# Optimization experiments

Hardware: AMD Instinct MI355X
Metric: run time of the kernel (lower is better)

## Reference

```python
import math
import jax, jax.numpy as jnp
import numpy as np

B, S, H, NH = 2, 2048, 1024, 4
DH = H // NH


def setup_inputs() -> dict:
    key = jax.random.key(0)
    ks = jax.random.split(key, 8)
    gate_std = 1.0 / math.sqrt(3 * H)
    return {
        "q": jax.random.normal(ks[0], (B, S, H), jnp.float32),
        "k": jax.random.normal(ks[1], (B, S, H), jnp.float32),
        "v": jax.random.normal(ks[2], (B, S, H), jnp.float32),
        "w_igate": jax.random.normal(ks[3], (NH, 3 * H), jnp.float32) * gate_std,
        "b_igate": jax.random.normal(ks[4], (NH,), jnp.float32) * 0.1,
        "w_fgate": jax.random.normal(ks[5], (NH, 3 * H), jnp.float32) * gate_std,
        "b_fgate": jnp.linspace(3.4, 6.0, NH, dtype=jnp.float32),  # bias_linspace_init_
        "ln_weight": jnp.zeros((H,), jnp.float32),  # residual weight: effective scale = 1 + w
    }


def _mlstm_parallel(qh, kh, vh, ig, fg, eps=1e-6):
    # qh,kh,vh: (B,NH,S,DH); ig,fg: (B,NH,S)
    b, nh, s, dh = qh.shape
    log_f = jax.nn.log_sigmoid(fg)                       # (B,NH,S)
    pcs = jnp.pad(jnp.cumsum(log_f, axis=-1), ((0, 0), (0, 0), (1, 0)))  # (B,NH,S+1)
    mat = pcs[..., :, None] - pcs[..., None, :]          # (B,NH,S+1,S+1)
    ltr = jnp.tril(jnp.ones((s, s), dtype=bool))
    log_fg_matrix = jnp.where(ltr, mat[..., 1:, 1:], -jnp.inf)
    log_D = log_fg_matrix + ig[..., None, :]             # (B,NH,S,S)
    max_log_D = jnp.max(log_D, axis=-1, keepdims=True)   # rowwise stabilization
    D = jnp.exp(log_D - max_log_D)
    qk = jnp.einsum('bhsd,bhtd->bhst', qh, kh) / math.sqrt(dh)
    C = qk * D
    normalizer = jnp.maximum(jnp.abs(C.sum(axis=-1, keepdims=True)), jnp.exp(-max_log_D))
    Cn = C / (normalizer + eps)
    return jnp.einsum('bhst,bhtd->bhsd', Cn, vh)         # (B,NH,S,DH)


def reference(q, k, v, w_igate, b_igate, w_fgate, b_fgate, ln_weight):
    b, s, h = q.shape
    nh = b_igate.shape[0]
    dh = h // nh
    # gate preactivations from concat([q,k,v])
    gin = jnp.concatenate([q, k, v], axis=-1)            # (B,S,3H)
    ig = jnp.einsum('bsd,hd->bhs', gin, w_igate) + b_igate[None, :, None]
    fg = jnp.einsum('bsd,hd->bhs', gin, w_fgate) + b_fgate[None, :, None]
    # split heads
    qh = q.reshape(b, s, nh, dh).transpose(0, 2, 1, 3)
    kh = k.reshape(b, s, nh, dh).transpose(0, 2, 1, 3)
    vh = v.reshape(b, s, nh, dh).transpose(0, 2, 1, 3)
    hst = _mlstm_parallel(qh, kh, vh, ig, fg)            # (B,NH,S,DH)
    # MultiHeadLayerNorm: group_norm over DH per head (biased variance), scale = 1 + ln_weight
    mean = hst.mean(axis=-1, keepdims=True)
    var = hst.var(axis=-1, keepdims=True)
    hn = (hst - mean) / jnp.sqrt(var + 1e-5)
    scale = (1.0 + ln_weight).reshape(nh, dh)
    hn = hn * scale[None, :, None, :]
    return hn.transpose(0, 2, 1, 3).reshape(b, s, h)
```

## Files before the change

kernel.cpp:

```cpp
#include <hip/hip_runtime.h>
#include <hip/hip_bf16.h>
#include <cstddef>

constexpr int Bx = 2, Sx = 2048, Hx = 1024, NHx = 4, DHx = 256;
constexpr float RSQ = 0.0625f;

typedef __attribute__((ext_vector_type(8))) short    bf16x8;
typedef __attribute__((ext_vector_type(4))) float    f32x4;

__device__ __forceinline__ float logsigf(float x) {
  return (x >= 0.0f) ? -log1pf(expf(-x)) : x - log1pf(expf(x));
}
__device__ __forceinline__ unsigned short f2bf(float x) {
  unsigned u = __builtin_bit_cast(unsigned, x);
  u = (u + 0x7fffu + ((u >> 16) & 1u)) >> 16;
  return (unsigned short)u;
}
__device__ __forceinline__ unsigned pk2bf(float a, float b) {
  return (unsigned)f2bf(a) | ((unsigned)f2bf(b) << 16);
}

__global__ __launch_bounds__(256)
void gates_kernel(const float* __restrict__ q, const float* __restrict__ k,
                  const float* __restrict__ v,
                  const float* __restrict__ wi, const float* __restrict__ bi,
                  const float* __restrict__ wf, const float* __restrict__ bf,
                  float* __restrict__ ig, float* __restrict__ fg,
                  unsigned short* __restrict__ Qb, unsigned short* __restrict__ Kb)
{
  const int bs = blockIdx.x;
  const int t  = threadIdx.x;
  const int b = bs >> 11, spos = bs & 2047;
  float p[8] = {0,0,0,0,0,0,0,0};
  const size_t rowoff = (size_t)bs * Hx;
  for (int idx = t; idx < 3 * Hx; idx += 256) {
    float gv;
    if (idx < Hx) {
      gv = q[rowoff + idx];
      Qb[((size_t)(b * NHx + (idx >> 8)) * Sx + spos) * DHx + (idx & 255)] = f2bf(gv);
    } else if (idx < 2 * Hx) {
      gv = k[rowoff + idx - Hx];
      int kd = idx - Hx;
      Kb[((size_t)(b * NHx + (kd >> 8)) * Sx + spos) * DHx + (kd & 255)] = f2bf(gv);
    } else {
      gv = v[rowoff + idx - 2 * Hx];
    }
#pragma unroll
    for (int h = 0; h < NHx; ++h) {
      p[h]     += gv * wi[h * 3 * Hx + idx];
      p[4 + h] += gv * wf[h * 3 * Hx + idx];
    }
  }
  __shared__ float red[8][256];
#pragma unroll
  for (int g2 = 0; g2 < 8; ++g2) red[g2][t] = p[g2];
  __syncthreads();
  for (int s2 = 128; s2 > 0; s2 >>= 1) {
    if (t < s2) {
#pragma unroll
      for (int g2 = 0; g2 < 8; ++g2) red[g2][t] += red[g2][t + s2];
    }
    __syncthreads();
  }
  if (t < 8) {
    const int h = t & 3;
    const size_t o = ((size_t)(b * NHx + h)) * Sx + spos;
    if (t < 4) ig[o] = red[t][0] + bi[h];
    else       fg[o] = red[t][0] + bf[h];
  }
}

__global__ __launch_bounds__(256)
void scan_kernel(const float* __restrict__ ig, const float* __restrict__ fg,
                 float* __restrict__ av, float* __restrict__ Mv,
                 float* __restrict__ nfv)
{
  const int bh = blockIdx.x;
  const int t  = threadIdx.x;
  const size_t base = (size_t)bh * Sx;
  const int s0 = t * 8;
  float4 f0 = *(const float4*)(fg + base + s0);
  float4 f1 = *(const float4*)(fg + base + s0 + 4);
  float4 g0 = *(const float4*)(ig + base + s0);
  float4 g1 = *(const float4*)(ig + base + s0 + 4);
  float xf[8] = {f0.x,f0.y,f0.z,f0.w,f1.x,f1.y,f1.z,f1.w};
  float xi[8] = {g0.x,g0.y,g0.z,g0.w,g1.x,g1.y,g1.z,g1.w};
  float ps[8];
  float run = 0.0f;
#pragma unroll
  for (int i = 0; i < 8; ++i) { run += logsigf(xf[i]); ps[i] = run; }
  __shared__ float ssum[256];
  __shared__ float smax[256];
  ssum[t] = run;
  __syncthreads();
  for (int st = 1; st < 256; st <<= 1) {
    float addv = (t >= st) ? ssum[t - st] : 0.0f;
    __syncthreads();
    ssum[t] += addv;
    __syncthreads();
  }
  const float exs = (t > 0) ? ssum[t - 1] : 0.0f;
  float a[8], pm[8];
  float rm = -INFINITY;
#pragma unroll
  for (int i = 0; i < 8; ++i) {
    a[i] = xi[i] - (exs + ps[i]);
    rm = fmaxf(rm, a[i]);
    pm[i] = rm;
  }
  smax[t] = rm;
  __syncthreads();
  for (int st = 1; st < 256; st <<= 1) {
    float mv = (t >= st) ? smax[t - st] : -INFINITY;
    __syncthreads();
    smax[t] = fmaxf(smax[t], mv);
    __syncthreads();
  }
  const float exm = (t > 0) ? smax[t - 1] : -INFINITY;
#pragma unroll
  for (int i = 0; i < 8; ++i) {
    const float M = fmaxf(exm, pm[i]);
    const float F = exs + ps[i];
    av[base + s0 + i]  = a[i];
    Mv[base + s0 + i]  = M;
    nfv[base + s0 + i] = expf(-(F + M));
  }
}

__global__ __launch_bounds__(256)
void vtrans_kernel(const float* __restrict__ v, unsigned short* __restrict__ vt)
{
  __shared__ float tile[64][68];
  const int st0 = blockIdx.x * 64, dt0 = blockIdx.y * 64;
  const int bh = blockIdx.z, b = bh >> 2, h = bh & 3;
  const int t = threadIdx.x;
#pragma unroll
  for (int i = 0; i < 4; ++i) {
    int u = t + 256 * i;
    int r = u >> 4, c4 = (u & 15) * 4;
    const float* p = v + ((size_t)(b * Sx) + st0 + r) * Hx + h * DHx + dt0 + c4;
    float4 vv = *(const float4*)p;
    tile[r][c4] = vv.x; tile[r][c4+1] = vv.y; tile[r][c4+2] = vv.z; tile[r][c4+3] = vv.w;
  }
  __syncthreads();
#pragma unroll
  for (int i = 0; i < 4; ++i) {
    int u = t + 256 * i;
    int dr = u >> 4, c4 = (u & 15) * 4;
    ushort4 o;
    o.x = f2bf(tile[c4+0][dr]); o.y = f2bf(tile[c4+1][dr]);
    o.z = f2bf(tile[c4+2][dr]); o.w = f2bf(tile[c4+3][dr]);
    *(ushort4*)(vt + ((size_t)bh * DHx + dt0 + dr) * Sx + st0 + c4) = o;
  }
}

constexpr int QSTR = 264;
constexpr int PSTR = 136;

__global__ __launch_bounds__(512, 4)
void mlstm_mfma(const unsigned short* __restrict__ Qb,
                const unsigned short* __restrict__ Kb,
                const unsigned short* __restrict__ Vt,
                const float* __restrict__ av, const float* __restrict__ Mv,
                const float* __restrict__ nfv, const float* __restrict__ lnw,
                float* __restrict__ out)
{
  __shared__ __align__(16) unsigned short Qls[32 * QSTR];
  __shared__ __align__(16) unsigned short Pls[2][32 * PSTR];
  __shared__ float red[8][2][16][3];

  const int bh = blockIdx.x, b = bh >> 2, h = bh & 3;
  const int ti = (int)gridDim.y - 1 - (int)blockIdx.y;
  const int i0 = ti * 32;
  const int tid = threadIdx.x;
  const int w = tid >> 6, l = tid & 63;
  const int lg = l >> 4, ll = l & 15;
  const size_t bhS = (size_t)bh * Sx;

  {
    const int r = tid >> 4, c = (tid & 15) * 16;
    const unsigned short* qp = Qb + (bhS + i0 + r) * DHx + c;
    bf16x8 v0 = *(const bf16x8*)qp;
    bf16x8 v1 = *(const bf16x8*)(qp + 8);
    *(bf16x8*)&Qls[r * QSTR + c] = v0;
    *(bf16x8*)&Qls[r * QSTR + c + 8] = v1;
  }
  float Mq[2], nfq[2];
#pragma unroll
  for (int qg = 0; qg < 2; ++qg) {
    Mq[qg]  = Mv[bhS + i0 + qg * 16 + ll];
    nfq[qg] = nfv[bhS + i0 + qg * 16 + ll];
  }
  f32x4 acc[2][2];
#pragma unroll
  for (int dt = 0; dt < 2; ++dt)
#pragma unroll
    for (int qg = 0; qg < 2; ++qg) acc[dt][qg] = f32x4{0, 0, 0, 0};
  float rsum[2] = {0.f, 0.f};
  __syncthreads();

  const int nt = (i0 + 32 + 127) >> 7;
  for (int tj = 0; tj < nt; ++tj) {
    const int j0 = tj << 7;
    const int kb = j0 + w * 16;
    bf16x8 kf[8];
    {
      const unsigned short* kp = Kb + (bhS + kb + ll) * DHx + lg * 8;
#pragma unroll
      for (int d8 = 0; d8 < 8; ++d8) kf[d8] = *(const bf16x8*)(kp + d8 * 32);
    }
    const f32x4 a4 = *(const f32x4*)(av + bhS + kb + lg * 4);
    f32x4 st0 = {0,0,0,0}, st1 = {0,0,0,0};
#pragma unroll
    for (int d8 = 0; d8 < 8; ++d8) {
      bf16x8 q0 = *(const bf16x8*)&Qls[ll * QSTR + d8 * 32 + lg * 8];
      bf16x8 q1 = *(const bf16x8*)&Qls[(16 + ll) * QSTR + d8 * 32 + lg * 8];
      st0 = __builtin_amdgcn_mfma_f32_16x16x32_bf16(kf[d8], q0, st0, 0, 0, 0);
      st1 = __builtin_amdgcn_mfma_f32_16x16x32_bf16(kf[d8], q1, st1, 0, 0, 0);
    }
#pragma unroll
    for (int qg = 0; qg < 2; ++qg) {
      const f32x4 s = qg ? st1 : st0;
      const int qrow = i0 + qg * 16 + ll;
      const int k0i = kb + lg * 4;
      float p0 = (k0i + 0 <= qrow) ? s[0] * (RSQ * __expf(a4[0] - Mq[qg])) : 0.f;
      float p1 = (k0i + 1 <= qrow) ? s[1] * (RSQ * __expf(a4[1] - Mq[qg])) : 0.f;
      float p2 = (k0i + 2 <= qrow) ? s[2] * (RSQ * __expf(a4[2] - Mq[qg])) : 0.f;
      float p3 = (k0i + 3 <= qrow) ? s[3] * (RSQ * __expf(a4[3] - Mq[qg])) : 0.f;
      rsum[qg] += (p0 + p1) + (p2 + p3);
      uint2 pk = make_uint2(pk2bf(p0, p1), pk2bf(p2, p3));
      *(uint2*)&Pls[tj & 1][(qg * 16 + ll) * PSTR + w * 16 + lg * 4] = pk;
    }
    __syncthreads();
    const unsigned short* vp = Vt + ((size_t)bh * DHx + w * 32 + ll) * Sx + j0 + lg * 8;
#pragma unroll
    for (int kap = 0; kap < 4; ++kap) {
      bf16x8 pf0 = *(const bf16x8*)&Pls[tj & 1][ll * PSTR + kap * 32 + lg * 8];
      bf16x8 pf1 = *(const bf16x8*)&Pls[tj & 1][(16 + ll) * PSTR + kap * 32 + lg * 8];
#pragma unroll
      for (int dt = 0; dt < 2; ++dt) {
        bf16x8 vf = *(const bf16x8*)(vp + (size_t)dt * 16 * Sx + kap * 32);
        acc[dt][0] = __builtin_amdgcn_mfma_f32_16x16x32_bf16(vf, pf0, acc[dt][0], 0, 0, 0);
        acc[dt][1] = __builtin_amdgcn_mfma_f32_16x16x32_bf16(vf, pf1, acc[dt][1], 0, 0, 0);
      }
    }
  }

#pragma unroll
  for (int qg = 0; qg < 2; ++qg) {
    float rs = rsum[qg];
    float s1 = 0.f, s2 = 0.f;
#pragma unroll
    for (int dt = 0; dt < 2; ++dt)
#pragma unroll
      for (int r = 0; r < 4; ++r) {
        const float x = acc[dt][qg][r];
        s1 += x; s2 += x * x;
      }
    rs += __shfl_xor(rs, 16); rs += __shfl_xor(rs, 32);
    s1 += __shfl_xor(s1, 16); s1 += __shfl_xor(s1, 32);
    s2 += __shfl_xor(s2, 16); s2 += __shfl_xor(s2, 32);
    if (l < 16) {
      red[w][qg][l][0] = rs;
      red[w][qg][l][1] = s1;
      red[w][qg][l][2] = s2;
    }
  }
  __syncthreads();

#pragma unroll
  for (int qg = 0; qg < 2; ++qg) {
    const int q = qg * 16 + ll;
    float rs = 0.f, s1 = 0.f, s2 = 0.f;
#pragma unroll
    for (int wj = 0; wj < 8; ++wj) {
      rs += red[wj][qg][ll][0];
      s1 += red[wj][qg][ll][1];
      s2 += red[wj][qg][ll][2];
    }
    const float inv = 1.f / (fmaxf(fabsf(rs), nfq[qg]) + 1e-6f);
    const float mean = s1 * inv * (1.f / 256.f);
    const float ex2  = s2 * inv * inv * (1.f / 256.f);
    const float var  = ex2 - mean * mean;
    const float rstd = rsqrtf(var + 1e-5f);
    float* op = out + ((size_t)b * Sx + i0 + q) * Hx + h * DHx;
#pragma unroll
    for (int dt = 0; dt < 2; ++dt) {
      const int dbase = w * 32 + dt * 16 + lg * 4;
      f32x4 lw = *(const f32x4*)(lnw + h * DHx + dbase);
      float4 o;
      o.x = (acc[dt][qg][0] * inv - mean) * rstd * (1.f + lw[0]);
      o.y = (acc[dt][qg][1] * inv - mean) * rstd * (1.f + lw[1]);
      o.z = (acc[dt][qg][2] * inv - mean) * rstd * (1.f + lw[2]);
      o.w = (acc[dt][qg][3] * inv - mean) * rstd * (1.f + lw[3]);
      *(float4*)(op + dbase) = o;
    }
  }
}

extern "C" void kernel_launch(void* const* d_in, const int* in_sizes, int n_in,
                              void* d_out, int out_size, void* d_ws, size_t ws_size,
                              hipStream_t stream) {
  const float* q   = (const float*)d_in[0];
  const float* k   = (const float*)d_in[1];
  const float* v   = (const float*)d_in[2];
  const float* wi  = (const float*)d_in[3];
  const float* bi  = (const float*)d_in[4];
  const float* wf  = (const float*)d_in[5];
  const float* bf  = (const float*)d_in[6];
  const float* lnw = (const float*)d_in[7];
  float* out = (float*)d_out;
  float* ws  = (float*)d_ws;

  const int G = Bx * NHx * Sx;
  float* ig  = ws;
  float* fg  = ws + (size_t)G;
  float* av  = ws + (size_t)2 * G;
  float* Mv  = ws + (size_t)3 * G;
  float* nfv = ws + (size_t)4 * G;
  unsigned short* Qb = (unsigned short*)(ws + (size_t)5 * G);
  unsigned short* Kb = Qb + (size_t)Bx * Sx * Hx;
  unsigned short* Vt = Kb + (size_t)Bx * Sx * Hx;

  gates_kernel<<<Bx * Sx, 256, 0, stream>>>(q, k, v, wi, bi, wf, bf, ig, fg, Qb, Kb);
  scan_kernel<<<Bx * NHx, 256, 0, stream>>>(ig, fg, av, Mv, nfv);
  dim3 gT(Sx / 64, DHx / 64, Bx * NHx);
  vtrans_kernel<<<gT, 256, 0, stream>>>(v, Vt);
  dim3 g4(Bx * NHx, Sx / 32);
  mlstm_mfma<<<g4, 512, 0, stream>>>(Qb, Kb, Vt, av, Mv, nfv, lnw, out);
}
```

Measured before the change: 134.7 us.

## Rework gates kernel vectorization and restructure mLSTM tile loop with K prefetch

The gates kernel now has each wavefront handle two rows with float4 loads, reusing each weight load across both rows and reducing with wave shuffles instead of a shared-memory tree. The main mLSTM kernel shrinks the key tile from 128 to 64 and splits the 8 waves into 4 key slices by 2 query halves. It double-buffers K fragments in registers, prefetching the next tile while softmax-like scaling runs, loads V fragments early, and raises wave priority around the MFMA sections. The aim is to hide global-load latency and trim wasted causal work at the diagonal, at the cost of twice as many barriers and more register pressure.

```diff
diff --git a/kernel.cpp b/kernel.cpp
--- a/kernel.cpp
+++ b/kernel.cpp
@@ -20,7 +20,7 @@
   return (unsigned)f2bf(a) | ((unsigned)f2bf(b) << 16);
 }
 
-__global__ __launch_bounds__(256)
+__global__ __launch_bounds__(512)
 void gates_kernel(const float* __restrict__ q, const float* __restrict__ k,
                   const float* __restrict__ v,
                   const float* __restrict__ wi, const float* __restrict__ bi,
@@ -28,45 +28,64 @@
                   float* __restrict__ ig, float* __restrict__ fg,
                   unsigned short* __restrict__ Qb, unsigned short* __restrict__ Kb)
 {
-  const int bs = blockIdx.x;
-  const int t  = threadIdx.x;
-  const int b = bs >> 11, spos = bs & 2047;
-  float p[8] = {0,0,0,0,0,0,0,0};
-  const size_t rowoff = (size_t)bs * Hx;
-  for (int idx = t; idx < 3 * Hx; idx += 256) {
-    float gv;
-    if (idx < Hx) {
-      gv = q[rowoff + idx];
-      Qb[((size_t)(b * NHx + (idx >> 8)) * Sx + spos) * DHx + (idx & 255)] = f2bf(gv);
-    } else if (idx < 2 * Hx) {
-      gv = k[rowoff + idx - Hx];
-      int kd = idx - Hx;
-      Kb[((size_t)(b * NHx + (kd >> 8)) * Sx + spos) * DHx + (kd & 255)] = f2bf(gv);
-    } else {
-      gv = v[rowoff + idx - 2 * Hx];
-    }
-#pragma unroll
-    for (int h = 0; h < NHx; ++h) {
-      p[h]     += gv * wi[h * 3 * Hx + idx];
-      p[4 + h] += gv * wf[h * 3 * Hx + idx];
-    }
-  }
-  __shared__ float red[8][256];
-#pragma unroll
-  for (int g2 = 0; g2 < 8; ++g2) red[g2][t] = p[g2];
-  __syncthreads();
-  for (int s2 = 128; s2 > 0; s2 >>= 1) {
-    if (t < s2) {
-#pragma unroll
-      for (int g2 = 0; g2 < 8; ++g2) red[g2][t] += red[g2][t + s2];
-    }
-    __syncthreads();
-  }
-  if (t < 8) {
-    const int h = t & 3;
-    const size_t o = ((size_t)(b * NHx + h)) * Sx + spos;
-    if (t < 4) ig[o] = red[t][0] + bi[h];
-    else       fg[o] = red[t][0] + bf[h];
+  const int w = threadIdx.x >> 6, l = threadIdx.x & 63;
+  const int bs0 = blockIdx.x * 16;
+  const int bsr0 = bs0 + w * 2, bsr1 = bsr0 + 1;
+  float p[2][8];
+#pragma unroll
+  for (int rr = 0; rr < 2; ++rr)
+#pragma unroll
+    for (int g2 = 0; g2 < 8; ++g2) p[rr][g2] = 0.f;
+
+#pragma unroll
+  for (int chunk = 0; chunk < 12; ++chunk) {
+    const int idx = l * 4 + chunk * 256;
+    const float* src; int off;
+    if (idx < 1024)       { src = q; off = idx; }
+    else if (idx < 2048)  { src = k; off = idx - 1024; }
+    else                  { src = v; off = idx - 2048; }
+    float4 g0 = *(const float4*)(src + (size_t)bsr0 * Hx + off);
+    float4 g1 = *(const float4*)(src + (size_t)bsr1 * Hx + off);
+#pragma unroll
+    for (int h = 0; h < 4; ++h) {
+      float4 wiv = *(const float4*)(wi + h * 3 * Hx + idx);
+      float4 wfv = *(const float4*)(wf + h * 3 * Hx + idx);
+      p[0][h]     += g0.x*wiv.x + g0.y*wiv.y + g0.z*wiv.z + g0.w*wiv.w;
+      p[1][h]     += g1.x*wiv.x + g1.y*wiv.y + g1.z*wiv.z + g1.w*wiv.w;
+      p[0][4 + h] += g0.x*wfv.x + g0.y*wfv.y + g0.z*wfv.z + g0.w*wfv.w;
+      p[1][4 + h] += g1.x*wfv.x + g1.y*wfv.y + g1.z*wfv.z + g1.w*wfv.w;
+    }
+    if (idx < 2048) {
+      unsigned short* dst = (idx < 1024) ? Qb : Kb;
+      const int hh = off >> 8, d = off & 255;
+      const int b0 = bsr0 >> 11, s0p = bsr0 & 2047;
+      const int b1 = bsr1 >> 11, s1p = bsr1 & 2047;
+      ushort4 o0; o0.x=f2bf(g0.x); o0.y=f2bf(g0.y); o0.z=f2bf(g0.z); o0.w=f2bf(g0.w);
+      ushort4 o1; o1.x=f2bf(g1.x); o1.y=f2bf(g1.y); o1.z=f2bf(g1.z); o1.w=f2bf(g1.w);
+      *(ushort4*)(dst + ((size_t)(b0 * NHx + hh) * Sx + s0p) * DHx + d) = o0;
+      *(ushort4*)(dst + ((size_t)(b1 * NHx + hh) * Sx + s1p) * DHx + d) = o1;
+    }
+  }
+#pragma unroll
+  for (int rr = 0; rr < 2; ++rr)
+#pragma unroll
+    for (int g2 = 0; g2 < 8; ++g2) {
+      float x = p[rr][g2];
+      x += __shfl_xor(x, 1);  x += __shfl_xor(x, 2);  x += __shfl_xor(x, 4);
+      x += __shfl_xor(x, 8);  x += __shfl_xor(x, 16); x += __shfl_xor(x, 32);
+      p[rr][g2] = x;
+    }
+  if (l == 0) {
+#pragma unroll
+    for (int rr = 0; rr < 2; ++rr) {
+      const int bs = bs0 + w * 2 + rr;
+      const int b = bs >> 11, spos = bs & 2047;
+#pragma unroll
+      for (int h = 0; h < 4; ++h) {
+        ig[(size_t)(b * NHx + h) * Sx + spos] = p[rr][h] + bi[h];
+        fg[(size_t)(b * NHx + h) * Sx + spos] = p[rr][4 + h] + bf[h];
+      }
+    }
   }
 }
 
@@ -155,7 +174,7 @@
 }
 
 constexpr int QSTR = 264;
-constexpr int PSTR = 136;
+constexpr int PSTR = 72;
 
 __global__ __launch_bounds__(512, 4)
 void mlstm_mfma(const unsigned short* __restrict__ Qb,
@@ -167,88 +186,102 @@
 {
   __shared__ __align__(16) unsigned short Qls[32 * QSTR];
   __shared__ __align__(16) unsigned short Pls[2][32 * PSTR];
-  __shared__ float red[8][2][16][3];
+  __shared__ float redRS[4][2][16];
+  __shared__ float redS[8][2][16][2];
 
   const int bh = blockIdx.x, b = bh >> 2, h = bh & 3;
   const int ti = (int)gridDim.y - 1 - (int)blockIdx.y;
   const int i0 = ti * 32;
   const int tid = threadIdx.x;
   const int w = tid >> 6, l = tid & 63;
+  const int ks = w & 3, qh = w >> 2;
   const int lg = l >> 4, ll = l & 15;
   const size_t bhS = (size_t)bh * Sx;
 
   {
     const int r = tid >> 4, c = (tid & 15) * 16;
     const unsigned short* qp = Qb + (bhS + i0 + r) * DHx + c;
-    bf16x8 v0 = *(const bf16x8*)qp;
-    bf16x8 v1 = *(const bf16x8*)(qp + 8);
-    *(bf16x8*)&Qls[r * QSTR + c] = v0;
-    *(bf16x8*)&Qls[r * QSTR + c + 8] = v1;
-  }
-  float Mq[2], nfq[2];
-#pragma unroll
-  for (int qg = 0; qg < 2; ++qg) {
-    Mq[qg]  = Mv[bhS + i0 + qg * 16 + ll];
-    nfq[qg] = nfv[bhS + i0 + qg * 16 + ll];
-  }
+    *(bf16x8*)&Qls[r * QSTR + c]     = *(const bf16x8*)qp;
+    *(bf16x8*)&Qls[r * QSTR + c + 8] = *(const bf16x8*)(qp + 8);
+  }
+  const float Mq = Mv[bhS + i0 + qh * 16 + ll];
+
   f32x4 acc[2][2];
 #pragma unroll
   for (int dt = 0; dt < 2; ++dt)
 #pragma unroll
     for (int qg = 0; qg < 2; ++qg) acc[dt][qg] = f32x4{0, 0, 0, 0};
-  float rsum[2] = {0.f, 0.f};
-  __syncthreads();
-
-  const int nt = (i0 + 32 + 127) >> 7;
-  for (int tj = 0; tj < nt; ++tj) {
-    const int j0 = tj << 7;
-    const int kb = j0 + w * 16;
-    bf16x8 kf[8];
-    {
-      const unsigned short* kp = Kb + (bhS + kb + ll) * DHx + lg * 8;
-#pragma unroll
-      for (int d8 = 0; d8 < 8; ++d8) kf[d8] = *(const bf16x8*)(kp + d8 * 32);
-    }
-    const f32x4 a4 = *(const f32x4*)(av + bhS + kb + lg * 4);
-    f32x4 st0 = {0,0,0,0}, st1 = {0,0,0,0};
+  float rsum = 0.f;
+  __syncthreads();
+
+  const int nt = (i0 + 32 + 63) >> 6;
+  const unsigned short* kbase = Kb + (bhS + ks * 16 + ll) * DHx + lg * 8;
+  const unsigned short* vbase = Vt + ((size_t)bh * DHx + w * 32 + ll) * Sx + lg * 8;
+
+  bf16x8 kA[8], kB[8];
+#pragma unroll
+  for (int d8 = 0; d8 < 8; ++d8) kA[d8] = *(const bf16x8*)(kbase + d8 * 32);
+
+  auto body = [&](int tj, bf16x8 (&kc)[8], bf16x8 (&kn)[8]) {
+    const int j0 = tj * 64;
+    f32x4 a4 = *(const f32x4*)(av + bhS + j0 + ks * 16 + lg * 4);
+    bf16x8 vf[2][2];
+#pragma unroll
+    for (int dt = 0; dt < 2; ++dt)
+#pragma unroll
+      for (int kap = 0; kap < 2; ++kap)
+        vf[dt][kap] = *(const bf16x8*)(vbase + (size_t)dt * 16 * Sx + j0 + kap * 32);
+    f32x4 st = {0, 0, 0, 0};
+    __builtin_amdgcn_s_setprio(1);
 #pragma unroll
     for (int d8 = 0; d8 < 8; ++d8) {
-      bf16x8 q0 = *(const bf16x8*)&Qls[ll * QSTR + d8 * 32 + lg * 8];
-      bf16x8 q1 = *(const bf16x8*)&Qls[(16 + ll) * QSTR + d8 * 32 + lg * 8];
-      st0 = __builtin_amdgcn_mfma_f32_16x16x32_bf16(kf[d8], q0, st0, 0, 0, 0);
-      st1 = __builtin_amdgcn_mfma_f32_16x16x32_bf16(kf[d8], q1, st1, 0, 0, 0);
-    }
-#pragma unroll
-    for (int qg = 0; qg < 2; ++qg) {
-      const f32x4 s = qg ? st1 : st0;
-      const int qrow = i0 + qg * 16 + ll;
-      const int k0i = kb + lg * 4;
-      float p0 = (k0i + 0 <= qrow) ? s[0] * (RSQ * __expf(a4[0] - Mq[qg])) : 0.f;
-      float p1 = (k0i + 1 <= qrow) ? s[1] * (RSQ * __expf(a4[1] - Mq[qg])) : 0.f;
-      float p2 = (k0i + 2 <= qrow) ? s[2] * (RSQ * __expf(a4[2] - Mq[qg])) : 0.f;
-      float p3 = (k0i + 3 <= qrow) ? s[3] * (RSQ * __expf(a4[3] - Mq[qg])) : 0.f;
-      rsum[qg] += (p0 + p1) + (p2 + p3);
-      uint2 pk = make_uint2(pk2bf(p0, p1), pk2bf(p2, p3));
-      *(uint2*)&Pls[tj & 1][(qg * 16 + ll) * PSTR + w * 16 + lg * 4] = pk;
-    }
-    __syncthreads();
-    const unsigned short* vp = Vt + ((size_t)bh * DHx + w * 32 + ll) * Sx + j0 + lg * 8;
-#pragma unroll
-    for (int kap = 0; kap < 4; ++kap) {
+      bf16x8 qf = *(const bf16x8*)&Qls[(qh * 16 + ll) * QSTR + d8 * 32 + lg * 8];
+      st = __builtin_amdgcn_mfma_f32_16x16x32_bf16(kc[d8], qf, st, 0, 0, 0);
+    }
+    __builtin_amdgcn_s_setprio(0);
+    const int tn = (tj + 1 < nt) ? (tj + 1) : tj;
+    const unsigned short* kp = kbase + ((size_t)tn * 64) * DHx;
+#pragma unroll
+    for (int d8 = 0; d8 < 8; ++d8) kn[d8] = *(const bf16x8*)(kp + d8 * 32);
+    const int qrow = i0 + qh * 16 + ll;
+    const int k0i = j0 + ks * 16 + lg * 4;
+    float p0 = (k0i + 0 <= qrow) ? st[0] * (RSQ * __expf(a4[0] - Mq)) : 0.f;
+    float p1 = (k0i + 1 <= qrow) ? st[1] * (RSQ * __expf(a4[1] - Mq)) : 0.f;
+    float p2 = (k0i + 2 <= qrow) ? st[2] * (RSQ * __expf(a4[2] - Mq)) : 0.f;
+    float p3 = (k0i + 3 <= qrow) ? st[3] * (RSQ * __expf(a4[3] - Mq)) : 0.f;
+    rsum += (p0 + p1) + (p2 + p3);
+    *(uint2*)&Pls[tj & 1][(qh * 16 + ll) * PSTR + ks * 16 + lg * 4] =
+        make_uint2(pk2bf(p0, p1), pk2bf(p2, p3));
+    __syncthreads();
+    __builtin_amdgcn_s_setprio(1);
+#pragma unroll
+    for (int kap = 0; kap < 2; ++kap) {
       bf16x8 pf0 = *(const bf16x8*)&Pls[tj & 1][ll * PSTR + kap * 32 + lg * 8];
       bf16x8 pf1 = *(const bf16x8*)&Pls[tj & 1][(16 + ll) * PSTR + kap * 32 + lg * 8];
 #pragma unroll
       for (int dt = 0; dt < 2; ++dt) {
-        bf16x8 vf = *(const bf16x8*)(vp + (size_t)dt * 16 * Sx + kap * 32);
-        acc[dt][0] = __builtin_amdgcn_mfma_f32_16x16x32_bf16(vf, pf0, acc[dt][0], 0, 0, 0);
-        acc[dt][1] = __builtin_amdgcn_mfma_f32_16x16x32_bf16(vf, pf1, acc[dt][1], 0, 0, 0);
+        acc[dt][0] = __builtin_amdgcn_mfma_f32_16x16x32_bf16(vf[dt][kap], pf0, acc[dt][0], 0, 0, 0);
+        acc[dt][1] = __builtin_amdgcn_mfma_f32_16x16x32_bf16(vf[dt][kap], pf1, acc[dt][1], 0, 0, 0);
       }
     }
-  }
-
+    __builtin_amdgcn_s_setprio(0);
+  };
+
+  int tj = 0;
+  while (true) {
+    body(tj, kA, kB);
+    if (++tj >= nt) break;
+    body(tj, kB, kA);
+    if (++tj >= nt) break;
+  }
+
+  {
+    float rs = rsum;
+    rs += __shfl_xor(rs, 16); rs += __shfl_xor(rs, 32);
+    if (l < 16) redRS[ks][qh][l] = rs;
+  }
 #pragma unroll
   for (int qg = 0; qg < 2; ++qg) {
-    float rs = rsum[qg];
     float s1 = 0.f, s2 = 0.f;
 #pragma unroll
     for (int dt = 0; dt < 2; ++dt)
@@ -257,28 +290,24 @@
         const float x = acc[dt][qg][r];
         s1 += x; s2 += x * x;
       }
-    rs += __shfl_xor(rs, 16); rs += __shfl_xor(rs, 32);
     s1 += __shfl_xor(s1, 16); s1 += __shfl_xor(s1, 32);
     s2 += __shfl_xor(s2, 16); s2 += __shfl_xor(s2, 32);
-    if (l < 16) {
-      red[w][qg][l][0] = rs;
-      red[w][qg][l][1] = s1;
-      red[w][qg][l][2] = s2;
-    }
+    if (l < 16) { redS[w][qg][l][0] = s1; redS[w][qg][l][1] = s2; }
   }
   __syncthreads();
 
 #pragma unroll
   for (int qg = 0; qg < 2; ++qg) {
     const int q = qg * 16 + ll;
-    float rs = 0.f, s1 = 0.f, s2 = 0.f;
+    float rs = redRS[0][qg][ll] + redRS[1][qg][ll] + redRS[2][qg][ll] + redRS[3][qg][ll];
+    float s1 = 0.f, s2 = 0.f;
 #pragma unroll
     for (int wj = 0; wj < 8; ++wj) {
-      rs += red[wj][qg][ll][0];
-      s1 += red[wj][qg][ll][1];
-      s2 += red[wj][qg][ll][2];
-    }
-    const float inv = 1.f / (fmaxf(fabsf(rs), nfq[qg]) + 1e-6f);
+      s1 += redS[wj][qg][ll][0];
+      s2 += redS[wj][qg][ll][1];
+    }
+    const float nf = nfv[bhS + i0 + q];
+    const float inv = 1.f / (fmaxf(fabsf(rs), nf) + 1e-6f);
     const float mean = s1 * inv * (1.f / 256.f);
     const float ex2  = s2 * inv * inv * (1.f / 256.f);
     const float var  = ex2 - mean * mean;
@@ -322,7 +351,7 @@
   unsigned short* Kb = Qb + (size_t)Bx * Sx * Hx;
   unsigned short* Vt = Kb + (size_t)Bx * Sx * Hx;
 
-  gates_kernel<<<Bx * Sx, 256, 0, stream>>>(q, k, v, wi, bi, wf, bf, ig, fg, Qb, Kb);
+  gates_kernel<<<Bx * Sx / 16, 512, 0, stream>>>(q, k, v, wi, bi, wf, bf, ig, fg, Qb, Kb);
   scan_kernel<<<Bx * NHx, 256, 0, stream>>>(ig, fg, av, Mv, nfv);
   dim3 gT(Sx / 64, DHx / 64, Bx * NHx);
   vtrans_kernel<<<gT, 256, 0, stream>>>(v, Vt);
```

Result: slower. 171.7 us, median of 2 (+27.5%).

## Restructure gates kernel to wave-per-two-rows and XOR-swizzle LDS tiles

Applied to the files above, without the earlier changes.

The gates kernel now runs 512-thread blocks that each handle 16 sequence rows, with each wavefront processing two rows using float4 loads. Gate weights are reused across the two rows, and the reduction uses wave shuffles instead of a shared-memory tree with many barriers. In the main MFMA kernel, the padded Q and P LDS strides are replaced by an XOR swizzle on 16-byte chunks. This keeps bank conflicts low while shrinking the LDS footprint. The risk is lower parallelism in the gates kernel (fewer blocks) and extra index arithmetic.

```diff
diff --git a/kernel.cpp b/kernel.cpp
--- a/kernel.cpp
+++ b/kernel.cpp
@@ -20,7 +20,7 @@
   return (unsigned)f2bf(a) | ((unsigned)f2bf(b) << 16);
 }
 
-__global__ __launch_bounds__(256)
+__global__ __launch_bounds__(512)
 void gates_kernel(const float* __restrict__ q, const float* __restrict__ k,
                   const float* __restrict__ v,
                   const float* __restrict__ wi, const float* __restrict__ bi,
@@ -28,45 +28,64 @@
                   float* __restrict__ ig, float* __restrict__ fg,
                   unsigned short* __restrict__ Qb, unsigned short* __restrict__ Kb)
 {
-  const int bs = blockIdx.x;
-  const int t  = threadIdx.x;
-  const int b = bs >> 11, spos = bs & 2047;
-  float p[8] = {0,0,0,0,0,0,0,0};
-  const size_t rowoff = (size_t)bs * Hx;
-  for (int idx = t; idx < 3 * Hx; idx += 256) {
-    float gv;
-    if (idx < Hx) {
-      gv = q[rowoff + idx];
-      Qb[((size_t)(b * NHx + (idx >> 8)) * Sx + spos) * DHx + (idx & 255)] = f2bf(gv);
-    } else if (idx < 2 * Hx) {
-      gv = k[rowoff + idx - Hx];
-      int kd = idx - Hx;
-      Kb[((size_t)(b * NHx + (kd >> 8)) * Sx + spos) * DHx + (kd & 255)] = f2bf(gv);
-    } else {
-      gv = v[rowoff + idx - 2 * Hx];
-    }
-#pragma unroll
-    for (int h = 0; h < NHx; ++h) {
-      p[h]     += gv * wi[h * 3 * Hx + idx];
-      p[4 + h] += gv * wf[h * 3 * Hx + idx];
-    }
-  }
-  __shared__ float red[8][256];
-#pragma unroll
-  for (int g2 = 0; g2 < 8; ++g2) red[g2][t] = p[g2];
-  __syncthreads();
-  for (int s2 = 128; s2 > 0; s2 >>= 1) {
-    if (t < s2) {
-#pragma unroll
-      for (int g2 = 0; g2 < 8; ++g2) red[g2][t] += red[g2][t + s2];
-    }
-    __syncthreads();
-  }
-  if (t < 8) {
-    const int h = t & 3;
-    const size_t o = ((size_t)(b * NHx + h)) * Sx + spos;
-    if (t < 4) ig[o] = red[t][0] + bi[h];
-    else       fg[o] = red[t][0] + bf[h];
+  const int w = threadIdx.x >> 6, l = threadIdx.x & 63;
+  const int bs0 = blockIdx.x * 16;
+  const int bsr0 = bs0 + w * 2, bsr1 = bsr0 + 1;
+  float p[2][8];
+#pragma unroll
+  for (int rr = 0; rr < 2; ++rr)
+#pragma unroll
+    for (int g2 = 0; g2 < 8; ++g2) p[rr][g2] = 0.f;
+
+#pragma unroll
+  for (int chunk = 0; chunk < 12; ++chunk) {
+    const int idx = l * 4 + chunk * 256;
+    const float* src; int off;
+    if (idx < 1024)       { src = q; off = idx; }
+    else if (idx < 2048)  { src = k; off = idx - 1024; }
+    else                  { src = v; off = idx - 2048; }
+    float4 g0 = *(const float4*)(src + (size_t)bsr0 * Hx + off);
+    float4 g1 = *(const float4*)(src + (size_t)bsr1 * Hx + off);
+#pragma unroll
+    for (int h = 0; h < 4; ++h) {
+      float4 wiv = *(const float4*)(wi + h * 3 * Hx + idx);
+      float4 wfv = *(const float4*)(wf + h * 3 * Hx + idx);
+      p[0][h]     += g0.x*wiv.x + g0.y*wiv.y + g0.z*wiv.z + g0.w*wiv.w;
+      p[1][h]     += g1.x*wiv.x + g1.y*wiv.y + g1.z*wiv.z + g1.w*wiv.w;
+      p[0][4 + h] += g0.x*wfv.x + g0.y*wfv.y + g0.z*wfv.z + g0.w*wfv.w;
+      p[1][4 + h] += g1.x*wfv.x + g1.y*wfv.y + g1.z*wfv.z + g1.w*wfv.w;
+    }
+    if (idx < 2048) {
+      unsigned short* dst = (idx < 1024) ? Qb : Kb;
+      const int hh = off >> 8, d = off & 255;
+      const int b0 = bsr0 >> 11, s0p = bsr0 & 2047;
+      const int b1 = bsr1 >> 11, s1p = bsr1 & 2047;
+      ushort4 o0; o0.x=f2bf(g0.x); o0.y=f2bf(g0.y); o0.z=f2bf(g0.z); o0.w=f2bf(g0.w);
+      ushort4 o1; o1.x=f2bf(g1.x); o1.y=f2bf(g1.y); o1.z=f2bf(g1.z); o1.w=f2bf(g1.w);
+      *(ushort4*)(dst + ((size_t)(b0 * NHx + hh) * Sx + s0p) * DHx + d) = o0;
+      *(ushort4*)(dst + ((size_t)(b1 * NHx + hh) * Sx + s1p) * DHx + d) = o1;
+    }
+  }
+#pragma unroll
+  for (int rr = 0; rr < 2; ++rr)
+#pragma unroll
+    for (int g2 = 0; g2 < 8; ++g2) {
+      float x = p[rr][g2];
+      x += __shfl_xor(x, 1);  x += __shfl_xor(x, 2);  x += __shfl_xor(x, 4);
+      x += __shfl_xor(x, 8);  x += __shfl_xor(x, 16); x += __shfl_xor(x, 32);
+      p[rr][g2] = x;
+    }
+  if (l == 0) {
+#pragma unroll
+    for (int rr = 0; rr < 2; ++rr) {
+      const int bs = bs0 + w * 2 + rr;
+      const int b = bs >> 11, spos = bs & 2047;
+#pragma unroll
+      for (int h = 0; h < 4; ++h) {
+        ig[(size_t)(b * NHx + h) * Sx + spos] = p[rr][h] + bi[h];
+        fg[(size_t)(b * NHx + h) * Sx + spos] = p[rr][4 + h] + bf[h];
+      }
+    }
   }
 }
 
@@ -154,9 +173,6 @@
   }
 }
 
-constexpr int QSTR = 264;
-constexpr int PSTR = 136;
-
 __global__ __launch_bounds__(512, 4)
 void mlstm_mfma(const unsigned short* __restrict__ Qb,
                 const unsigned short* __restrict__ Kb,
@@ -165,8 +181,8 @@
                 const float* __restrict__ nfv, const float* __restrict__ lnw,
                 float* __restrict__ out)
 {
-  __shared__ __align__(16) unsigned short Qls[32 * QSTR];
-  __shared__ __align__(16) unsigned short Pls[2][32 * PSTR];
+  __shared__ __align__(16) unsigned short Qls[32 * 256];
+  __shared__ __align__(16) unsigned short Pls[2][32 * 128];
   __shared__ float red[8][2][16][3];
 
   const int bh = blockIdx.x, b = bh >> 2, h = bh & 3;
@@ -178,12 +194,10 @@
   const size_t bhS = (size_t)bh * Sx;
 
   {
-    const int r = tid >> 4, c = (tid & 15) * 16;
-    const unsigned short* qp = Qb + (bhS + i0 + r) * DHx + c;
-    bf16x8 v0 = *(const bf16x8*)qp;
-    bf16x8 v1 = *(const bf16x8*)(qp + 8);
-    *(bf16x8*)&Qls[r * QSTR + c] = v0;
-    *(bf16x8*)&Qls[r * QSTR + c + 8] = v1;
+    const int r = tid >> 4, ch0 = (tid & 15) * 2;
+    const unsigned short* qp = Qb + (bhS + i0 + r) * DHx + ch0 * 8;
+    *(bf16x8*)&Qls[r * 256 + ((ch0 ^ (r & 7)) << 3)]       = *(const bf16x8*)qp;
+    *(bf16x8*)&Qls[r * 256 + (((ch0 + 1) ^ (r & 7)) << 3)] = *(const bf16x8*)(qp + 8);
   }
   float Mq[2], nfq[2];
 #pragma unroll
@@ -213,8 +227,9 @@
     f32x4 st0 = {0,0,0,0}, st1 = {0,0,0,0};
 #pragma unroll
     for (int d8 = 0; d8 < 8; ++d8) {
-      bf16x8 q0 = *(const bf16x8*)&Qls[ll * QSTR + d8 * 32 + lg * 8];
-      bf16x8 q1 = *(const bf16x8*)&Qls[(16 + ll) * QSTR + d8 * 32 + lg * 8];
+      const int ph = ((4 * d8 + lg) ^ (ll & 7)) << 3;
+      bf16x8 q0 = *(const bf16x8*)&Qls[ll * 256 + ph];
+      bf16x8 q1 = *(const bf16x8*)&Qls[(16 + ll) * 256 + ph];
       st0 = __builtin_amdgcn_mfma_f32_16x16x32_bf16(kf[d8], q0, st0, 0, 0, 0);
       st1 = __builtin_amdgcn_mfma_f32_16x16x32_bf16(kf[d8], q1, st1, 0, 0, 0);
     }
@@ -229,14 +244,16 @@
       float p3 = (k0i + 3 <= qrow) ? s[3] * (RSQ * __expf(a4[3] - Mq[qg])) : 0.f;
       rsum[qg] += (p0 + p1) + (p2 + p3);
       uint2 pk = make_uint2(pk2bf(p0, p1), pk2bf(p2, p3));
-      *(uint2*)&Pls[tj & 1][(qg * 16 + ll) * PSTR + w * 16 + lg * 4] = pk;
+      const int pc = (((2 * w + (lg >> 1)) ^ (ll & 7)) << 3) + ((lg & 1) << 2);
+      *(uint2*)&Pls[tj & 1][(qg * 16 + ll) * 128 + pc] = pk;
     }
     __syncthreads();
     const unsigned short* vp = Vt + ((size_t)bh * DHx + w * 32 + ll) * Sx + j0 + lg * 8;
 #pragma unroll
     for (int kap = 0; kap < 4; ++kap) {
-      bf16x8 pf0 = *(const bf16x8*)&Pls[tj & 1][ll * PSTR + kap * 32 + lg * 8];
-      bf16x8 pf1 = *(const bf16x8*)&Pls[tj & 1][(16 + ll) * PSTR + kap * 32 + lg * 8];
+      const int pc = ((4 * kap + lg) ^ (ll & 7)) << 3;
+      bf16x8 pf0 = *(const bf16x8*)&Pls[tj & 1][ll * 128 + pc];
+      bf16x8 pf1 = *(const bf16x8*)&Pls[tj & 1][(16 + ll) * 128 + pc];
 #pragma unroll
       for (int dt = 0; dt < 2; ++dt) {
         bf16x8 vf = *(const bf16x8*)(vp + (size_t)dt * 16 * Sx + kap * 32);
@@ -322,7 +339,7 @@
   unsigned short* Kb = Qb + (size_t)Bx * Sx * Hx;
   unsigned short* Vt = Kb + (size_t)Bx * Sx * Hx;
 
-  gates_kernel<<<Bx * Sx, 256, 0, stream>>>(q, k, v, wi, bi, wf, bf, ig, fg, Qb, Kb);
+  gates_kernel<<<Bx * Sx / 16, 512, 0, stream>>>(q, k, v, wi, bi, wf, bf, ig, fg, Qb, Kb);
   scan_kernel<<<Bx * NHx, 256, 0, stream>>>(ig, fg, av, Mv, nfv);
   dim3 gT(Sx / 64, DHx / 64, Bx * NHx);
   vtrans_kernel<<<gT, 256, 0, stream>>>(v, Vt);
```

New measurement: 126.8 us. 5.9% less time.
